# Kernel tuning notes

Hardware: AMD Instinct MI355X
Metric: run time of the kernel (lower is better)

The kernel has to match this reference:

```python
import jax, jax.numpy as jnp
import numpy as np

N = 4096
IN_DIM = 512
NUM_HEADS = 8
SUB_DIM = 64
ETA = 0.5
LAMBDA_SPARSE = 0.1
EDGE_PROB = 0.01


def setup_inputs() -> dict:
    key = jax.random.key(0)
    k_h, k_u, k_a = jax.random.split(key, 3)
    H = jax.random.normal(k_h, (N, IN_DIM), dtype=jnp.float32)
    # Per-head orthonormal subspace bases (QR init, as in the torch module)
    raw = jax.random.normal(k_u, (NUM_HEADS, IN_DIM, SUB_DIM), dtype=jnp.float32)
    U = jax.vmap(lambda a: jnp.linalg.qr(a)[0])(raw)  # [K, in_dim, r]
    # Binary adjacency mask with self-loops (float 0/1)
    adj = (jax.random.uniform(k_a, (N, N)) < EDGE_PROB).astype(jnp.float32)
    adj_mask = jnp.maximum(adj, jnp.eye(N, dtype=jnp.float32))
    threshold = jnp.full((IN_DIM,), LAMBDA_SPARSE, dtype=jnp.float32)
    return {"H": H, "adj_mask": adj_mask, "U": U, "threshold": threshold}


def reference(H, adj_mask, U, threshold):
    r = U.shape[-1]
    scale = jnp.asarray(r, H.dtype) ** 0.5
    # Z_k = U_k^T H^T  -> [K, r, n]
    Z = jnp.einsum('kdr,nd->krn', U, H)
    # scores[k, i, j] = Z_k[:, i] . Z_k[:, j] / sqrt(r), masked to neighbors
    scores = jnp.einsum('kri,krj->kij', Z, Z) / scale
    scores = scores + (1.0 - adj_mask) * (-1e9)
    alpha = jax.nn.softmax(scores, axis=-1)          # [K, n, n]
    # Z_agg[k, :, i] = sum_j alpha[k, i, j] * Z_k[:, j]
    Z_agg = jnp.einsum('krj,kij->kri', Z, alpha)      # [K, r, n]
    # project back and sum heads: [n, d]
    agg = jnp.einsum('kdr,kri->id', U, Z_agg)
    H_half = H + ETA * agg
    H_out = jax.nn.relu(H_half - threshold[None, :])
    # orthogonality loss: sum_{k<l} ||U_k^T U_l||_F^2
    gram = jnp.einsum('kdr,lds->klrs', U, U)
    sq = jnp.sum(gram ** 2, axis=(-1, -2))            # [K, K]
    orth_loss = 0.5 * (jnp.sum(sq) - jnp.trace(sq))
    return H_out, orth_loss
```

## Files before the change

### kernel.cpp

```cpp
#include <hip/hip_runtime.h>
#include <hip/hip_bf16.h>

#define NN   4096
#define DD   512
#define KH   8
#define RR   64
#define CAP  128

typedef unsigned short u16;
typedef unsigned int   u32;
typedef unsigned long long u64;
typedef __attribute__((ext_vector_type(8))) short short8;
typedef __attribute__((ext_vector_type(4))) float f32x4;

__device__ __forceinline__ float bflo(u32 v){ union{u32 i; float f;} c; c.i = v << 16;        return c.f; }
__device__ __forceinline__ float bfhi(u32 v){ union{u32 i; float f;} c; c.i = v & 0xFFFF0000u; return c.f; }
__device__ __forceinline__ u16 f2bf(float f){ __hip_bfloat16 h = __float2bfloat16(f); return *reinterpret_cast<u16*>(&h); }

__global__ __launch_bounds__(256) void prep_scan(const float* __restrict__ H, const float* __restrict__ U,
                                                 const float* __restrict__ adj,
                                                 u16* __restrict__ Hb, u16* __restrict__ Bt1,
                                                 u16* __restrict__ Bt2,
                                                 int* __restrict__ nlist, int* __restrict__ cnt,
                                                 float* __restrict__ lossP) {
    union SH {
        float tile[64][65];
        struct { float UkT[32][20]; float UlT[32][68]; } o;
    };
    __shared__ SH sh;
    __shared__ float red4[4];
    const int b = blockIdx.x, t = threadIdx.x;

    if (b < 112) {
        const int ob = b;
        const int pb = ob >> 2, strip = ob & 3;
        int idx = pb, k = 0, lh = 1;
        #pragma unroll
        for (int kk = 0; kk < 8; kk++) {
            int c = 7 - kk;
            if (idx < c) { k = kk; lh = kk + 1 + idx; break; }
            idx -= c;
        }
        const int r = t & 15;
        const int s0 = (t >> 4) * 4;
        const int r0g = strip * 16;
        const float* Uk = U + (size_t)k  * DD * RR;
        const float* Ul = U + (size_t)lh * DD * RR;
        float a0 = 0.f, a1 = 0.f, a2 = 0.f, a3 = 0.f;
        for (int dc = 0; dc < DD; dc += 32) {
            if (t < 128) {
                int dd = t >> 2, rq = t & 3;
                *(float4*)&sh.o.UkT[dd][rq * 4] = *(const float4*)(Uk + (size_t)(dc + dd) * RR + r0g + rq * 4);
            }
            #pragma unroll
            for (int s = 0; s < 2; s++) {
                int u = t + 256 * s;
                int dd = u >> 4, sq = u & 15;
                *(float4*)&sh.o.UlT[dd][sq * 4] = *(const float4*)(Ul + (size_t)(dc + dd) * RR + sq * 4);
            }
            __syncthreads();
            #pragma unroll 4
            for (int dd = 0; dd < 32; dd++) {
                float a = sh.o.UkT[dd][r];
                float4 bv = *(const float4*)&sh.o.UlT[dd][s0];
                a0 += a * bv.x; a1 += a * bv.y; a2 += a * bv.z; a3 += a * bv.w;
            }
            __syncthreads();
        }
        float v = a0 * a0 + a1 * a1 + a2 * a2 + a3 * a3;
        #pragma unroll
        for (int off = 32; off; off >>= 1) v += __shfl_down(v, off, 64);
        if ((t & 63) == 0) red4[t >> 6] = v;
        __syncthreads();
        if (t == 0) lossP[ob] = red4[0] + red4[1] + red4[2] + red4[3];
        return;
    }
    if (b < 176) {
        const int b2 = b - 112;
        const int k = b2 >> 3, d0 = (b2 & 7) * 64;
        #pragma unroll
        for (int s = 0; s < 4; s++) {
            int u = t + 256 * s;
            int dd = u >> 4, rq = u & 15;
            float4 v = *(const float4*)(U + ((size_t)(k * DD + d0 + dd)) * RR + rq * 4);
            sh.tile[dd][rq * 4 + 0] = v.x; sh.tile[dd][rq * 4 + 1] = v.y;
            sh.tile[dd][rq * 4 + 2] = v.z; sh.tile[dd][rq * 4 + 3] = v.w;
        }
        __syncthreads();
        {   int r = t >> 2;
            #pragma unroll
            for (int ii = 0; ii < 16; ii++) {
                int dd = (t & 3) * 16 + ii;
                Bt1[(size_t)(k * RR + r) * DD + d0 + dd] = f2bf(sh.tile[dd][r]);
            }
        }
        {   int dd = t >> 2, rb = (t & 3) * 16;
            #pragma unroll
            for (int ii = 0; ii < 16; ii++) {
                Bt2[(size_t)(d0 + dd) * DD + k * RR + rb + ii] = f2bf(sh.tile[dd][rb + ii]);
            }
        }
        return;
    }
    if (b < 1200) {
        const int row = (b - 176) * 4 + (t >> 6);
        const int lane = t & 63;
        const float* arow = adj + (size_t)row * NN;
        int* ndst = nlist + (size_t)row * CAP;
        const u64 lt = (1ull << lane) - 1;
        int base = 0;
        #pragma unroll
        for (int h = 0; h < 2; h++) {
            float4 mv[8];
            #pragma unroll
            for (int c = 0; c < 8; c++)
                mv[c] = *(const float4*)(arow + (h * 8 + c) * 256 + lane * 4);
            #pragma unroll
            for (int c = 0; c < 8; c++) {
                const int j = (h * 8 + c) * 256 + lane * 4;
                const u64 bx = __ballot(mv[c].x != 0.f);
                const u64 by = __ballot(mv[c].y != 0.f);
                const u64 bz = __ballot(mv[c].z != 0.f);
                const u64 bw = __ballot(mv[c].w != 0.f);
                const int nx = __popcll(bx), ny = __popcll(by), nz = __popcll(bz);
                if (mv[c].x != 0.f) { int p = base + __popcll(bx & lt);                if (p < CAP) ndst[p] = j;     }
                if (mv[c].y != 0.f) { int p = base + nx + __popcll(by & lt);           if (p < CAP) ndst[p] = j + 1; }
                if (mv[c].z != 0.f) { int p = base + nx + ny + __popcll(bz & lt);      if (p < CAP) ndst[p] = j + 2; }
                if (mv[c].w != 0.f) { int p = base + nx + ny + nz + __popcll(bw & lt); if (p < CAP) ndst[p] = j + 3; }
                base += nx + ny + nz + __popcll(bw);
            }
        }
        if (lane == 0) cnt[row] = min(base, CAP);
        return;
    }
    size_t id = (size_t)(b - 1200) * 256 + t;
    float4 v = *(const float4*)(H + id * 4);
    ushort4 o; o.x = f2bf(v.x); o.y = f2bf(v.y); o.z = f2bf(v.z); o.w = f2bf(v.w);
    *(ushort4*)(Hb + id * 4) = o;
}

__global__ __launch_bounds__(256) void zgemm_mfma(const u16* __restrict__ Hb, const u16* __restrict__ Bt1,
                                                  u16* __restrict__ Zb) {
    __shared__ short As[64][72];
    __shared__ short Bs[64][72];
    const int t = threadIdx.x;
    const int i0 = blockIdx.x * 64, n0 = blockIdx.y * 64;
    const int w = t >> 6, lane = t & 63;
    const int lm = lane & 15, lg = lane >> 4;
    f32x4 acc[4] = {};
    for (int kc = 0; kc < DD; kc += 64) {
        #pragma unroll
        for (int s = 0; s < 2; s++) {
            int c = t + 256 * s; int row = c >> 3, g = c & 7;
            *(short8*)&As[row][g * 8] = *(const short8*)(Hb  + (size_t)(i0 + row) * DD + kc + g * 8);
            *(short8*)&Bs[row][g * 8] = *(const short8*)(Bt1 + (size_t)(n0 + row) * DD + kc + g * 8);
        }
        __syncthreads();
        #pragma unroll
        for (int ks = 0; ks < 64; ks += 32) {
            short8 af = *(const short8*)&As[w * 16 + lm][ks + lg * 8];
            #pragma unroll
            for (int b = 0; b < 4; b++) {
                short8 bfr = *(const short8*)&Bs[b * 16 + lm][ks + lg * 8];
                acc[b] = __builtin_amdgcn_mfma_f32_16x16x32_bf16(af, bfr, acc[b], 0, 0, 0);
            }
        }
        __syncthreads();
    }
    #pragma unroll
    for (int b = 0; b < 4; b++)
        #pragma unroll
        for (int q = 0; q < 4; q++) {
            int row = i0 + w * 16 + lg * 4 + q;
            int col = n0 + b * 16 + lm;
            Zb[(size_t)row * DD + col] = f2bf(acc[b][q]);
        }
}

__global__ __launch_bounds__(512) void attn11(const u16* __restrict__ Zb, const int* __restrict__ nlist,
                                              const int* __restrict__ cnt, u16* __restrict__ Zaggb) {
    const int i = blockIdx.x, t = threadIdx.x;
    const int w = t >> 6, lane = t & 63;
    __shared__ int   nbrS[CAP];
    __shared__ float red[KH][DD];
    __shared__ float lS[KH][KH + 1];
    const int ci = cnt[i];
    if (t < CAP) nbrS[t] = nlist[(size_t)i * CAP + min(t, ci - 1)];
    __syncthreads();

    float a[8];
    {
        uint4 av = *(const uint4*)(Zb + (size_t)i * DD + lane * 8);
        a[0] = bflo(av.x); a[1] = bfhi(av.x); a[2] = bflo(av.y); a[3] = bfhi(av.y);
        a[4] = bflo(av.z); a[5] = bfhi(av.z); a[6] = bflo(av.w); a[7] = bfhi(av.w);
    }

    float l = 0.f;
    float acc[8] = {};
    const int nIt = (ci + 7) >> 3;

    uint4 b0 = *(const uint4*)(Zb + (size_t)nbrS[w] * DD + lane * 8);
    uint4 b1 = *(const uint4*)(Zb + (size_t)nbrS[min(w + 8, CAP - 1)] * DD + lane * 8);

    #define PROCESS(c, val)                                                        \
    {   float zf[8];                                                               \
        zf[0] = bflo(c.x); zf[1] = bfhi(c.x); zf[2] = bflo(c.y); zf[3] = bfhi(c.y);\
        zf[4] = bflo(c.z); zf[5] = bfhi(c.z); zf[6] = bflo(c.w); zf[7] = bfhi(c.w);\
        float s = zf[0]*a[0] + zf[1]*a[1] + zf[2]*a[2] + zf[3]*a[3]                \
                + zf[4]*a[4] + zf[5]*a[5] + zf[6]*a[6] + zf[7]*a[7];               \
        s += __shfl_xor(s, 1); s += __shfl_xor(s, 2); s += __shfl_xor(s, 4);       \
        const float e = (val) ? __expf(s * 0.125f) : 0.f;                          \
        l += e;                                                                    \
        _Pragma("unroll")                                                          \
        for (int d = 0; d < 8; d++) acc[d] += e * zf[d];                           \
    }

    for (int tt = 0; tt < nIt; tt += 2) {
        {   const uint4 c = b0;
            const int pf = min(w + 8 * (tt + 2), CAP - 1);
            b0 = *(const uint4*)(Zb + (size_t)nbrS[pf] * DD + lane * 8);
            const bool val = (w + 8 * tt) < ci;
            PROCESS(c, val);
        }
        if (tt + 1 < nIt) {
            const uint4 c = b1;
            const int pf = min(w + 8 * (tt + 3), CAP - 1);
            b1 = *(const uint4*)(Zb + (size_t)nbrS[pf] * DD + lane * 8);
            const bool val = (w + 8 * (tt + 1)) < ci;
            PROCESS(c, val);
        }
    }
    #undef PROCESS

    *(float4*)&red[w][lane * 8]     = make_float4(acc[0], acc[1], acc[2], acc[3]);
    *(float4*)&red[w][lane * 8 + 4] = make_float4(acc[4], acc[5], acc[6], acc[7]);
    if ((lane & 7) == 0) lS[w][lane >> 3] = l;
    __syncthreads();

    const int d = t, k = d >> 6;
    float ls = 0.f, sum = 0.f;
    #pragma unroll
    for (int ww = 0; ww < KH; ww++) { ls += lS[ww][k]; sum += red[ww][d]; }
    Zaggb[(size_t)i * DD + d] = f2bf(sum / ls);
}

__global__ __launch_bounds__(256) void outgemm_mfma(const u16* __restrict__ Ab, const u16* __restrict__ Btb,
                                                    const float* __restrict__ H, const float* __restrict__ thr,
                                                    const float* __restrict__ lossP,
                                                    float* __restrict__ out) {
    __shared__ short As[64][72];
    __shared__ short Bs[64][72];
    const int t = threadIdx.x;
    const int i0 = blockIdx.x * 64, n0 = blockIdx.y * 64;
    if (i0 == 0 && n0 == 0 && t < 64) {
        float v = lossP[t] + ((t + 64 < 112) ? lossP[t + 64] : 0.f);
        #pragma unroll
        for (int off = 32; off; off >>= 1) v += __shfl_down(v, off, 64);
        if (t == 0) out[(size_t)NN * DD] = v;
    }
    const int w = t >> 6, lane = t & 63;
    const int lm = lane & 15, lg = lane >> 4;
    f32x4 acc[4] = {};
    for (int kc = 0; kc < DD; kc += 64) {
        #pragma unroll
        for (int s = 0; s < 2; s++) {
            int c = t + 256 * s; int row = c >> 3, g = c & 7;
            *(short8*)&As[row][g * 8] = *(const short8*)(Ab  + (size_t)(i0 + row) * DD + kc + g * 8);
            *(short8*)&Bs[row][g * 8] = *(const short8*)(Btb + (size_t)(n0 + row) * DD + kc + g * 8);
        }
        __syncthreads();
        #pragma unroll
        for (int ks = 0; ks < 64; ks += 32) {
            short8 af = *(const short8*)&As[w * 16 + lm][ks + lg * 8];
            #pragma unroll
            for (int b = 0; b < 4; b++) {
                short8 bfr = *(const short8*)&Bs[b * 16 + lm][ks + lg * 8];
                acc[b] = __builtin_amdgcn_mfma_f32_16x16x32_bf16(af, bfr, acc[b], 0, 0, 0);
            }
        }
        __syncthreads();
    }
    #pragma unroll
    for (int b = 0; b < 4; b++) {
        const int col = n0 + b * 16 + lm;
        const float th = thr[col];
        #pragma unroll
        for (int q = 0; q < 4; q++) {
            int row = i0 + w * 16 + lg * 4 + q;
            float h = H[(size_t)row * DD + col];
            out[(size_t)row * DD + col] = fmaxf(h + 0.5f * acc[b][q] - th, 0.f);
        }
    }
}

extern "C" void kernel_launch(void* const* d_in, const int* in_sizes, int n_in,
                              void* d_out, int out_size, void* d_ws, size_t ws_size,
                              hipStream_t stream) {
    const float* H   = (const float*)d_in[0];
    const float* adj = (const float*)d_in[1];
    const float* U   = (const float*)d_in[2];
    const float* thr = (const float*)d_in[3];
    float* out = (float*)d_out;

    char* ws = (char*)d_ws;
    float* lossP = (float*)ws;
    u16*   Hb    = (u16*)(ws + 1024);
    u16*   Zb    = (u16*)(ws + 1024 + 4u * 1024 * 1024);
    u16*   Zaggb = (u16*)(ws + 1024 + 8u * 1024 * 1024);
    u16*   Bt1   = (u16*)(ws + 1024 + 12u * 1024 * 1024);
    u16*   Bt2   = (u16*)(ws + 1024 + 12u * 1024 * 1024 + 512u * 1024);
    int*   nlist = (int*)(ws + 1024 + 13u * 1024 * 1024);
    int*   cnt   = (int*)(ws + 1024 + 15u * 1024 * 1024 + 512u * 1024);

    prep_scan<<<3248, 256, 0, stream>>>(H, U, adj, Hb, Bt1, Bt2, nlist, cnt, lossP);
    zgemm_mfma<<<dim3(64, 8), 256, 0, stream>>>(Hb, Bt1, Zb);
    attn11<<<NN, 512, 0, stream>>>(Zb, nlist, cnt, Zaggb);
    outgemm_mfma<<<dim3(64, 8), 256, 0, stream>>>(Zaggb, Bt2, H, thr, lossP, out);
}
```

Measured before the change: 157.1 us.

## Fuse adjacency neighbor scan into attention kernel, drop neighbor list buffer

Moves the adjacency-row compaction out of the prep kernel and into the attention kernel. Each block now ballots over its own 4096-entry mask row, prefix-sums the per-wave counts in shared memory and builds the neighbor list directly in LDS. This removes the nlist/cnt global write and read-back and shrinks the prep grid. The cost is that the 64 MB adjacency read now sits inside the attention kernel, adding a block barrier and scan latency before the gathers start. The memory-bound scan no longer overlaps with the independent prep work.

```diff
diff --git a/kernel.cpp b/kernel.cpp
--- a/kernel.cpp
+++ b/kernel.cpp
@@ -18,10 +18,8 @@
 __device__ __forceinline__ u16 f2bf(float f){ __hip_bfloat16 h = __float2bfloat16(f); return *reinterpret_cast<u16*>(&h); }
 
 __global__ __launch_bounds__(256) void prep_scan(const float* __restrict__ H, const float* __restrict__ U,
-                                                 const float* __restrict__ adj,
                                                  u16* __restrict__ Hb, u16* __restrict__ Bt1,
                                                  u16* __restrict__ Bt2,
-                                                 int* __restrict__ nlist, int* __restrict__ cnt,
                                                  float* __restrict__ lossP) {
     union SH {
         float tile[64][65];
@@ -102,38 +100,7 @@
         }
         return;
     }
-    if (b < 1200) {
-        const int row = (b - 176) * 4 + (t >> 6);
-        const int lane = t & 63;
-        const float* arow = adj + (size_t)row * NN;
-        int* ndst = nlist + (size_t)row * CAP;
-        const u64 lt = (1ull << lane) - 1;
-        int base = 0;
-        #pragma unroll
-        for (int h = 0; h < 2; h++) {
-            float4 mv[8];
-            #pragma unroll
-            for (int c = 0; c < 8; c++)
-                mv[c] = *(const float4*)(arow + (h * 8 + c) * 256 + lane * 4);
-            #pragma unroll
-            for (int c = 0; c < 8; c++) {
-                const int j = (h * 8 + c) * 256 + lane * 4;
-                const u64 bx = __ballot(mv[c].x != 0.f);
-                const u64 by = __ballot(mv[c].y != 0.f);
-                const u64 bz = __ballot(mv[c].z != 0.f);
-                const u64 bw = __ballot(mv[c].w != 0.f);
-                const int nx = __popcll(bx), ny = __popcll(by), nz = __popcll(bz);
-                if (mv[c].x != 0.f) { int p = base + __popcll(bx & lt);                if (p < CAP) ndst[p] = j;     }
-                if (mv[c].y != 0.f) { int p = base + nx + __popcll(by & lt);           if (p < CAP) ndst[p] = j + 1; }
-                if (mv[c].z != 0.f) { int p = base + nx + ny + __popcll(bz & lt);      if (p < CAP) ndst[p] = j + 2; }
-                if (mv[c].w != 0.f) { int p = base + nx + ny + nz + __popcll(bw & lt); if (p < CAP) ndst[p] = j + 3; }
-                base += nx + ny + nz + __popcll(bw);
-            }
-        }
-        if (lane == 0) cnt[row] = min(base, CAP);
-        return;
-    }
-    size_t id = (size_t)(b - 1200) * 256 + t;
+    const size_t id = (size_t)(b - 176) * 256 + t;
     float4 v = *(const float4*)(H + id * 4);
     ushort4 o; o.x = f2bf(v.x); o.y = f2bf(v.y); o.z = f2bf(v.z); o.w = f2bf(v.w);
     *(ushort4*)(Hb + id * 4) = o;
@@ -177,16 +144,43 @@
         }
 }
 
-__global__ __launch_bounds__(512) void attn11(const u16* __restrict__ Zb, const int* __restrict__ nlist,
-                                              const int* __restrict__ cnt, u16* __restrict__ Zaggb) {
+__global__ __launch_bounds__(512) void attn12(const u16* __restrict__ Zb, const float* __restrict__ adj,
+                                              u16* __restrict__ Zaggb) {
     const int i = blockIdx.x, t = threadIdx.x;
     const int w = t >> 6, lane = t & 63;
     __shared__ int   nbrS[CAP];
+    __shared__ int   wbase[8];
     __shared__ float red[KH][DD];
     __shared__ float lS[KH][KH + 1];
-    const int ci = cnt[i];
-    if (t < CAP) nbrS[t] = nlist[(size_t)i * CAP + min(t, ci - 1)];
-    __syncthreads();
+
+    int tot = 0;
+    {
+        const float* arow = adj + (size_t)i * NN;
+        const float4 m0 = *(const float4*)(arow + t * 8);
+        const float4 m1 = *(const float4*)(arow + t * 8 + 4);
+        const float vals[8] = {m0.x, m0.y, m0.z, m0.w, m1.x, m1.y, m1.z, m1.w};
+        u64 bal[8];
+        #pragma unroll
+        for (int c = 0; c < 8; c++) bal[c] = __ballot(vals[c] != 0.f);
+        int cum[8], wcnt = 0;
+        #pragma unroll
+        for (int c = 0; c < 8; c++) { cum[c] = wcnt; wcnt += (int)__popcll(bal[c]); }
+        if (lane == 0) wbase[w] = wcnt;
+        __syncthreads();
+        int base = 0;
+        #pragma unroll
+        for (int ww = 0; ww < 8; ww++) { int v = wbase[ww]; if (ww < w) base += v; tot += v; }
+        const u64 lt = (1ull << lane) - 1;
+        #pragma unroll
+        for (int c = 0; c < 8; c++) {
+            if (vals[c] != 0.f) {
+                int p = base + cum[c] + (int)__popcll(bal[c] & lt);
+                if (p < CAP) nbrS[p] = t * 8 + c;
+            }
+        }
+        __syncthreads();
+    }
+    const int ci = min(tot, CAP);
 
     float a[8];
     {
@@ -199,8 +193,8 @@
     float acc[8] = {};
     const int nIt = (ci + 7) >> 3;
 
-    uint4 b0 = *(const uint4*)(Zb + (size_t)nbrS[w] * DD + lane * 8);
-    uint4 b1 = *(const uint4*)(Zb + (size_t)nbrS[min(w + 8, CAP - 1)] * DD + lane * 8);
+    uint4 b0 = *(const uint4*)(Zb + (size_t)nbrS[min(w, ci - 1)] * DD + lane * 8);
+    uint4 b1 = *(const uint4*)(Zb + (size_t)nbrS[min(w + 8, ci - 1)] * DD + lane * 8);
 
     #define PROCESS(c, val)                                                        \
     {   float zf[8];                                                               \
@@ -217,14 +211,14 @@
 
     for (int tt = 0; tt < nIt; tt += 2) {
         {   const uint4 c = b0;
-            const int pf = min(w + 8 * (tt + 2), CAP - 1);
+            const int pf = min(w + 8 * (tt + 2), ci - 1);
             b0 = *(const uint4*)(Zb + (size_t)nbrS[pf] * DD + lane * 8);
             const bool val = (w + 8 * tt) < ci;
             PROCESS(c, val);
         }
         if (tt + 1 < nIt) {
             const uint4 c = b1;
-            const int pf = min(w + 8 * (tt + 3), CAP - 1);
+            const int pf = min(w + 8 * (tt + 3), ci - 1);
             b1 = *(const uint4*)(Zb + (size_t)nbrS[pf] * DD + lane * 8);
             const bool val = (w + 8 * (tt + 1)) < ci;
             PROCESS(c, val);
@@ -309,11 +303,9 @@
     u16*   Zaggb = (u16*)(ws + 1024 + 8u * 1024 * 1024);
     u16*   Bt1   = (u16*)(ws + 1024 + 12u * 1024 * 1024);
     u16*   Bt2   = (u16*)(ws + 1024 + 12u * 1024 * 1024 + 512u * 1024);
-    int*   nlist = (int*)(ws + 1024 + 13u * 1024 * 1024);
-    int*   cnt   = (int*)(ws + 1024 + 15u * 1024 * 1024 + 512u * 1024);
-
-    prep_scan<<<3248, 256, 0, stream>>>(H, U, adj, Hb, Bt1, Bt2, nlist, cnt, lossP);
+
+    prep_scan<<<2224, 256, 0, stream>>>(H, U, Hb, Bt1, Bt2, lossP);
     zgemm_mfma<<<dim3(64, 8), 256, 0, stream>>>(Hb, Bt1, Zb);
-    attn11<<<NN, 512, 0, stream>>>(Zb, nlist, cnt, Zaggb);
+    attn12<<<NN, 512, 0, stream>>>(Zb, adj, Zaggb);
     outgemm_mfma<<<dim3(64, 8), 256, 0, stream>>>(Zaggb, Bt2, H, thr, lossP, out);
 }
```

New measurement: 160.5 us. 2.2% more time.

## Move adjacency scan into Z GEMM kernel to overlap memory and compute

Applied to the files above, without the earlier changes.

The adjacency-row scan that builds neighbor lists moves out of the prep kernel and into the Z GEMM launch. Blocks are interleaved two scan blocks per GEMM block, so the bandwidth-bound 64MB mask read can run alongside the MFMA tiles. The attention kernel's prefetch indices are also clamped to the actual neighbor count instead of CAP, so it stops reading stale list entries. The interleaving depends on the scheduler mixing block types well, and the GEMM grid is flattened from 2D to 1D.

```diff
diff --git a/kernel.cpp b/kernel.cpp
--- a/kernel.cpp
+++ b/kernel.cpp
@@ -18,10 +18,8 @@
 __device__ __forceinline__ u16 f2bf(float f){ __hip_bfloat16 h = __float2bfloat16(f); return *reinterpret_cast<u16*>(&h); }
 
 __global__ __launch_bounds__(256) void prep_scan(const float* __restrict__ H, const float* __restrict__ U,
-                                                 const float* __restrict__ adj,
                                                  u16* __restrict__ Hb, u16* __restrict__ Bt1,
                                                  u16* __restrict__ Bt2,
-                                                 int* __restrict__ nlist, int* __restrict__ cnt,
                                                  float* __restrict__ lossP) {
     union SH {
         float tile[64][65];
@@ -102,8 +100,23 @@
         }
         return;
     }
-    if (b < 1200) {
-        const int row = (b - 176) * 4 + (t >> 6);
+    const size_t id = (size_t)(b - 176) * 256 + t;
+    float4 v = *(const float4*)(H + id * 4);
+    ushort4 o; o.x = f2bf(v.x); o.y = f2bf(v.y); o.z = f2bf(v.z); o.w = f2bf(v.w);
+    *(ushort4*)(Hb + id * 4) = o;
+}
+
+__global__ __launch_bounds__(256) void zgemm_scan(const u16* __restrict__ Hb, const u16* __restrict__ Bt1,
+                                                  u16* __restrict__ Zb,
+                                                  const float* __restrict__ adj,
+                                                  int* __restrict__ nlist, int* __restrict__ cnt) {
+    __shared__ short As[64][72];
+    __shared__ short Bs[64][72];
+    const int b = blockIdx.x, t = threadIdx.x;
+
+    if (b % 3 != 2) {
+        const int sg = (b / 3) * 2 + (b % 3);
+        const int row = sg * 4 + (t >> 6);
         const int lane = t & 63;
         const float* arow = adj + (size_t)row * NN;
         int* ndst = nlist + (size_t)row * CAP;
@@ -133,47 +146,38 @@
         if (lane == 0) cnt[row] = min(base, CAP);
         return;
     }
-    size_t id = (size_t)(b - 1200) * 256 + t;
-    float4 v = *(const float4*)(H + id * 4);
-    ushort4 o; o.x = f2bf(v.x); o.y = f2bf(v.y); o.z = f2bf(v.z); o.w = f2bf(v.w);
-    *(ushort4*)(Hb + id * 4) = o;
-}
-
-__global__ __launch_bounds__(256) void zgemm_mfma(const u16* __restrict__ Hb, const u16* __restrict__ Bt1,
-                                                  u16* __restrict__ Zb) {
-    __shared__ short As[64][72];
-    __shared__ short Bs[64][72];
-    const int t = threadIdx.x;
-    const int i0 = blockIdx.x * 64, n0 = blockIdx.y * 64;
+
+    const int g = b / 3;
+    const int i0 = (g & 63) * 64, n0 = (g >> 6) * 64;
     const int w = t >> 6, lane = t & 63;
     const int lm = lane & 15, lg = lane >> 4;
     f32x4 acc[4] = {};
     for (int kc = 0; kc < DD; kc += 64) {
         #pragma unroll
         for (int s = 0; s < 2; s++) {
-            int c = t + 256 * s; int row = c >> 3, g = c & 7;
-            *(short8*)&As[row][g * 8] = *(const short8*)(Hb  + (size_t)(i0 + row) * DD + kc + g * 8);
-            *(short8*)&Bs[row][g * 8] = *(const short8*)(Bt1 + (size_t)(n0 + row) * DD + kc + g * 8);
+            int c = t + 256 * s; int row = c >> 3, gg = c & 7;
+            *(short8*)&As[row][gg * 8] = *(const short8*)(Hb  + (size_t)(i0 + row) * DD + kc + gg * 8);
+            *(short8*)&Bs[row][gg * 8] = *(const short8*)(Bt1 + (size_t)(n0 + row) * DD + kc + gg * 8);
         }
         __syncthreads();
         #pragma unroll
         for (int ks = 0; ks < 64; ks += 32) {
             short8 af = *(const short8*)&As[w * 16 + lm][ks + lg * 8];
             #pragma unroll
-            for (int b = 0; b < 4; b++) {
-                short8 bfr = *(const short8*)&Bs[b * 16 + lm][ks + lg * 8];
-                acc[b] = __builtin_amdgcn_mfma_f32_16x16x32_bf16(af, bfr, acc[b], 0, 0, 0);
+            for (int bb = 0; bb < 4; bb++) {
+                short8 bfr = *(const short8*)&Bs[bb * 16 + lm][ks + lg * 8];
+                acc[bb] = __builtin_amdgcn_mfma_f32_16x16x32_bf16(af, bfr, acc[bb], 0, 0, 0);
             }
         }
         __syncthreads();
     }
     #pragma unroll
-    for (int b = 0; b < 4; b++)
+    for (int bb = 0; bb < 4; bb++)
         #pragma unroll
         for (int q = 0; q < 4; q++) {
             int row = i0 + w * 16 + lg * 4 + q;
-            int col = n0 + b * 16 + lm;
-            Zb[(size_t)row * DD + col] = f2bf(acc[b][q]);
+            int col = n0 + bb * 16 + lm;
+            Zb[(size_t)row * DD + col] = f2bf(acc[bb][q]);
         }
 }
 
@@ -199,8 +203,8 @@
     float acc[8] = {};
     const int nIt = (ci + 7) >> 3;
 
-    uint4 b0 = *(const uint4*)(Zb + (size_t)nbrS[w] * DD + lane * 8);
-    uint4 b1 = *(const uint4*)(Zb + (size_t)nbrS[min(w + 8, CAP - 1)] * DD + lane * 8);
+    uint4 b0 = *(const uint4*)(Zb + (size_t)nbrS[min(w, ci - 1)] * DD + lane * 8);
+    uint4 b1 = *(const uint4*)(Zb + (size_t)nbrS[min(w + 8, ci - 1)] * DD + lane * 8);
 
     #define PROCESS(c, val)                                                        \
     {   float zf[8];                                                               \
@@ -217,14 +221,14 @@
 
     for (int tt = 0; tt < nIt; tt += 2) {
         {   const uint4 c = b0;
-            const int pf = min(w + 8 * (tt + 2), CAP - 1);
+            const int pf = min(w + 8 * (tt + 2), ci - 1);
             b0 = *(const uint4*)(Zb + (size_t)nbrS[pf] * DD + lane * 8);
             const bool val = (w + 8 * tt) < ci;
             PROCESS(c, val);
         }
         if (tt + 1 < nIt) {
             const uint4 c = b1;
-            const int pf = min(w + 8 * (tt + 3), CAP - 1);
+            const int pf = min(w + 8 * (tt + 3), ci - 1);
             b1 = *(const uint4*)(Zb + (size_t)nbrS[pf] * DD + lane * 8);
             const bool val = (w + 8 * (tt + 1)) < ci;
             PROCESS(c, val);
@@ -312,8 +316,8 @@
     int*   nlist = (int*)(ws + 1024 + 13u * 1024 * 1024);
     int*   cnt   = (int*)(ws + 1024 + 15u * 1024 * 1024 + 512u * 1024);
 
-    prep_scan<<<3248, 256, 0, stream>>>(H, U, adj, Hb, Bt1, Bt2, nlist, cnt, lossP);
-    zgemm_mfma<<<dim3(64, 8), 256, 0, stream>>>(Hb, Bt1, Zb);
+    prep_scan<<<2224, 256, 0, stream>>>(H, U, Hb, Bt1, Bt2, lossP);
+    zgemm_scan<<<1536, 256, 0, stream>>>(Hb, Bt1, Zb, adj, nlist, cnt);
     attn11<<<NN, 512, 0, stream>>>(Zb, nlist, cnt, Zaggb);
     outgemm_mfma<<<dim3(64, 8), 256, 0, stream>>>(Zaggb, Bt2, H, thr, lossP, out);
 }
```

Measured after the change: 162.4 us. 3.4% more time.
